# Optimization experiments

Hardware: AMD Instinct MI355X
Metric: run time of the kernel (lower is better)

## Reference

```python
import jax, jax.numpy as jnp
import numpy as np

IN_FEATURES = 3
HIDDEN = 32
NUM_LAYERS = 3
BATCH = 16384
NQ = 128


def setup_inputs() -> dict:
    key = jax.random.key(0)
    ks = jax.random.split(key, 12)
    x = jax.random.normal(ks[0], (BATCH, NQ, IN_FEATURES), dtype=jnp.float32)
    # adjacency with self-loops, row-normalised so each row sums to 1
    a = jax.random.uniform(ks[1], (NQ, NQ), dtype=jnp.float32)
    a = a + jnp.eye(NQ, dtype=jnp.float32)
    adj = a / jnp.sum(a, axis=1, keepdims=True)
    s_lift = 1.0 / np.sqrt(IN_FEATURES)
    s_hid = 1.0 / np.sqrt(HIDDEN)
    W_lift = jax.random.uniform(ks[2], (IN_FEATURES, HIDDEN), jnp.float32, -s_lift, s_lift)
    b_lift = jax.random.uniform(ks[3], (HIDDEN,), jnp.float32, -s_lift, s_lift)
    # stacked per-layer MLP params: [num_layers, ...]
    W1 = jax.random.uniform(ks[4], (NUM_LAYERS, HIDDEN, HIDDEN), jnp.float32, -s_hid, s_hid)
    b1 = jax.random.uniform(ks[5], (NUM_LAYERS, HIDDEN), jnp.float32, -s_hid, s_hid)
    W2 = jax.random.uniform(ks[6], (NUM_LAYERS, HIDDEN, HIDDEN), jnp.float32, -s_hid, s_hid)
    b2 = jax.random.uniform(ks[7], (NUM_LAYERS, HIDDEN), jnp.float32, -s_hid, s_hid)
    W_ro = jax.random.uniform(ks[8], (HIDDEN, 1), jnp.float32, -s_hid, s_hid)
    b_ro = jax.random.uniform(ks[9], (1,), jnp.float32, -s_hid, s_hid)
    return {"x": x, "adj": adj, "W_lift": W_lift, "b_lift": b_lift,
            "W1": W1, "b1": b1, "W2": W2, "b2": b2,
            "W_ro": W_ro, "b_ro": b_ro}


def reference(x, adj, W_lift, b_lift, W1, b1, W2, b2, W_ro, b_ro):
    # lift: [B, N, in] -> [B, N, H]
    h = x @ W_lift + b_lift
    for l in range(W1.shape[0]):  # small fixed layer count
        # local MLP: Linear -> ReLU -> (Dropout: identity at eval) -> Linear
        local = jnp.maximum(h @ W1[l] + b1[l], 0.0) @ W2[l] + b2[l]
        # dense adjacency aggregation: [N,N] x [B,N,H] -> [B,N,H]
        h = jnp.einsum('ij,bjk->bik', adj, local)
    graph_repr = jnp.mean(h, axis=1)  # [B, H]
    return graph_repr @ W_ro + b_ro   # [B, 1]
```

## Files before the change

### kernel.cpp

```cpp
#include <hip/hip_runtime.h>


typedef _Float16 f16;
typedef __attribute__((ext_vector_type(8))) _Float16 half8;
typedef __attribute__((ext_vector_type(4))) _Float16 half4;
typedef __attribute__((ext_vector_type(2))) __fp16 fp16x2;
typedef __attribute__((ext_vector_type(4))) float f32x4;

namespace {
constexpr int N = 128, H = 32;
constexpr int WS_ADJB = 0;
constexpr int WS_W0B  = 32768;
constexpr int WS_MB   = 33792;
constexpr int WS_BIAS = 37888;
constexpr int WS_V    = 38400;
constexpr int WS_U    = 38912;
constexpr int WS_C    = 39040;
}

static __device__ __forceinline__ half4 pk4(float a, float b, float c, float d) {
  union { half4 v; fp16x2 h[2]; } u;
  u.h[0] = __builtin_amdgcn_cvt_pkrtz(a, b);
  u.h[1] = __builtin_amdgcn_cvt_pkrtz(c, d);
  return u.v;
}
static __device__ __forceinline__ half4 relupk(f32x4 c) {
  const half4 z = {};
  return __builtin_elementwise_max(pk4(c[0], c[1], c[2], c[3]), z);
}
static __device__ __forceinline__ half4 pkc(f32x4 c) {
  return pk4(c[0], c[1], c[2], c[3]);
}
static __device__ __forceinline__ half8 cat(half4 lo, half4 hi) {
  return __builtin_shufflevector(lo, hi, 0, 1, 2, 3, 4, 5, 6, 7);
}

#define MF(A, B, C)   __builtin_amdgcn_mfma_f32_16x16x16f16((A), (B), (C), 0, 0, 0)
#define MF32(A, B, C) __builtin_amdgcn_mfma_f32_16x16x32_f16((A), (B), (C), 0, 0, 0)

__global__ void prep(const float* __restrict__ adj,
                     const float* __restrict__ W_lift,
                     const float* __restrict__ b_lift,
                     const float* __restrict__ W1,
                     const float* __restrict__ b1,
                     const float* __restrict__ W2,
                     const float* __restrict__ b2,
                     const float* __restrict__ W_ro,
                     const float* __restrict__ b_ro,
                     char* __restrict__ ws) {
  const int tid = threadIdx.x;
  f16* adjb  = (f16*)(ws + WS_ADJB);
  f16* w0b   = (f16*)(ws + WS_W0B);
  f16* mb    = (f16*)(ws + WS_MB);
  float* bia = (float*)(ws + WS_BIAS);
  float* v   = (float*)(ws + WS_V);
  float* u   = (float*)(ws + WS_U);
  float* cp  = (float*)(ws + WS_C);

  if (blockIdx.x != 0) {
    const int e = (blockIdx.x - 1) * 256 + tid;
    const int gi = e >> 8, c = (e >> 6) & 3, lane = e & 63;
    const int lr = lane & 15, q = lane >> 4;
    const float* src = adj + (gi * 16 + lr) * N + c * 32;
    f16* dst = adjb + e * 8;
#pragma unroll
    for (int j = 0; j < 8; ++j) {
      const int col = (j < 4) ? (4 * q + j) : (12 + 4 * q + j);
      dst[j] = (f16)src[col];
    }
    return;
  }

  __shared__ float tmp[3][H][H];
  __shared__ float vpart[2][N];
  {
    const int c = tid & 127, h = tid >> 7;
    float s = 0.f;
    for (int i = h * 64; i < h * 64 + 64; ++i) s += adj[i * N + c];
    vpart[h][c] = s;
  }
  for (int idx = tid; idx < 3 * H * H; idx += 256) {
    const int l = idx >> 10, rem = idx & 1023;
    const int k = rem >> 5, fo = rem & 31;
    float val = 0.f;
    if (l == 0) {
      if (k < 3) for (int c = 0; c < H; ++c) val += W_lift[k * H + c] * W1[c * H + fo];
    } else {
      const float* w2l = W2 + (l - 1) * H * H;
      const float* w1n = W1 + l * H * H;
      for (int c = 0; c < H; ++c) val += w2l[k * H + c] * w1n[c * H + fo];
    }
    tmp[l][k][fo] = val;
  }
  if (tid < H) {
    float s0 = b1[tid], s1 = b1[H + tid], s2 = b1[2 * H + tid];
    for (int c = 0; c < H; ++c) {
      s0 += b_lift[c] * W1[c * H + tid];
      s1 += b2[c] * W1[H * H + c * H + tid];
      s2 += b2[H + c] * W1[2 * H * H + c * H + tid];
    }
    bia[tid] = s0; bia[H + tid] = s1; bia[2 * H + tid] = s2;
    float su = 0.f;
    for (int c = 0; c < H; ++c) su += W2[2 * H * H + tid * H + c] * W_ro[c];
    u[tid] = su;
  }
  __syncthreads();
  if (tid < N) v[tid] = (vpart[0][tid] + vpart[1][tid]) * (1.0f / N);
  for (int e = tid; e < 512; e += 256) {
    const int t = e >> 8, lane = (e >> 2) & 63, j = e & 3;
    const int lr = lane & 15, q = lane >> 4;
    w0b[e] = (f16)tmp[0][q * 4 + j][t * 16 + lr];
  }
  for (int e = tid; e < 2048; e += 256) {
    const int l = e >> 10, rem = e & 1023;
    const int t = rem >> 9, lane = (rem >> 3) & 63, j = rem & 7;
    const int lr = lane & 15, q = lane >> 4;
    const int k = (j < 4) ? (4 * q + j) : (12 + 4 * q + j);
    mb[e] = (f16)tmp[1 + l][k][t * 16 + lr];
  }
  __syncthreads();
  if (tid < 64) {
    float s = (vpart[0][tid] + vpart[1][tid] + vpart[0][64 + tid] + vpart[1][64 + tid])
              * (1.0f / N);
#pragma unroll
    for (int off = 32; off > 0; off >>= 1) s += __shfl_down(s, off, 64);
    if (tid == 0) {
      float c2r = 0.f;
      for (int k = 0; k < H; ++k) c2r += b2[2 * H + k] * W_ro[k];
      cp[0] = c2r * s + b_ro[0];
    }
  }
}

__global__ __launch_bounds__(256, 2)
void gnn_mfma(const float* __restrict__ x,
              const char* __restrict__ ws,
              float* __restrict__ out) {
  const f16* adjb  = (const f16*)(ws + WS_ADJB);
  const f16* w0b   = (const f16*)(ws + WS_W0B);
  const f16* mb    = (const f16*)(ws + WS_MB);
  const float* bia = (const float*)(ws + WS_BIAS);
  const float* v   = (const float*)(ws + WS_V);
  const float* u   = (const float*)(ws + WS_U);
  const float* cp  = (const float*)(ws + WS_C);

  const int tid  = threadIdx.x;
  const int wave = tid >> 6;
  const int lane = tid & 63;
  const int lrow = lane & 15;
  const int quad = lane >> 4;
  const int b0   = blockIdx.x * 8 + wave * 2;
  const int b1   = b0 + 1;

  const f32x4 zero = {0.f, 0.f, 0.f, 0.f};

  half8 caA0, caA1, caA2, caA3, cbA0, cbA1, cbA2, cbA3;
  half8 caB0, caB1, caB2, caB3, cbB0, cbB1, cbB2, cbB3;
  half8 pfA0, pfA1, pfA2, pfA3, pfA4, pfA5, pfA6, pfA7;
  half8 pfB0, pfB1, pfB2, pfB3, pfB4, pfB5, pfB6, pfB7;

  {
    const half4 w0 = *(const half4*)(w0b + (0 * 64 + lane) * 4);
    const half4 w1 = *(const half4*)(w0b + (1 * 64 + lane) * 4);
    const float bb0 = bia[lrow], bb1 = bia[16 + lrow];
    const f32x4 bi0 = {bb0, bb0, bb0, bb0};
    const f32x4 bi1 = {bb1, bb1, bb1, bb1};
#define L0PAIR(g, CAA, CBA, CAB, CBB)                                        \
    {                                                                        \
      half4 xA0 = {}, xA1 = {}, xB0 = {}, xB1 = {};                          \
      if (quad == 0) {                                                       \
        const float* ra0 = x + ((size_t)b0 * N + (g) * 16 + lrow) * 3;       \
        const float* ra1 = x + ((size_t)b0 * N + ((g) + 1) * 16 + lrow) * 3; \
        const float* rb0 = x + ((size_t)b1 * N + (g) * 16 + lrow) * 3;       \
        const float* rb1 = x + ((size_t)b1 * N + ((g) + 1) * 16 + lrow) * 3; \
        xA0 = pk4(ra0[0], ra0[1], ra0[2], 0.f);                              \
        xA1 = pk4(ra1[0], ra1[1], ra1[2], 0.f);                              \
        xB0 = pk4(rb0[0], rb0[1], rb0[2], 0.f);                              \
        xB1 = pk4(rb1[0], rb1[1], rb1[2], 0.f);                              \
      }                                                                      \
      CAA = cat(relupk(MF(xA0, w0, bi0)), relupk(MF(xA1, w0, bi0)));         \
      CBA = cat(relupk(MF(xA0, w1, bi1)), relupk(MF(xA1, w1, bi1)));         \
      CAB = cat(relupk(MF(xB0, w0, bi0)), relupk(MF(xB1, w0, bi0)));         \
      CBB = cat(relupk(MF(xB0, w1, bi1)), relupk(MF(xB1, w1, bi1)));         \
    }
    L0PAIR(0, caA0, cbA0, caB0, cbB0) L0PAIR(2, caA1, cbA1, caB1, cbB1)
    L0PAIR(4, caA2, cbA2, caB2, cbB2) L0PAIR(6, caA3, cbA3, caB3, cbB3)
#undef L0PAIR
  }

#define GSTEP(gi, PFA, PFB)                                                  \
  {                                                                          \
    f32x4 aA0 = zero, aA1 = zero, aB0 = zero, aB1 = zero;                    \
    const f16* ab = adjb + ((gi) * 256 + lane) * 8;                          \
    half8 bt;                                                                \
    __builtin_amdgcn_s_setprio(1);                                           \
    bt = *(const half8*)(ab + 0 * 512);                                      \
    aA0 = MF32(caA0, bt, aA0); aA1 = MF32(cbA0, bt, aA1);                    \
    aB0 = MF32(caB0, bt, aB0); aB1 = MF32(cbB0, bt, aB1);                    \
    bt = *(const half8*)(ab + 1 * 512);                                      \
    aA0 = MF32(caA1, bt, aA0); aA1 = MF32(cbA1, bt, aA1);                    \
    aB0 = MF32(caB1, bt, aB0); aB1 = MF32(cbB1, bt, aB1);                    \
    bt = *(const half8*)(ab + 2 * 512);                                      \
    aA0 = MF32(caA2, bt, aA0); aA1 = MF32(cbA2, bt, aA1);                    \
    aB0 = MF32(caB2, bt, aB0); aB1 = MF32(cbB2, bt, aB1);                    \
    bt = *(const half8*)(ab + 3 * 512);                                      \
    aA0 = MF32(caA3, bt, aA0); aA1 = MF32(cbA3, bt, aA1);                    \
    aB0 = MF32(caB3, bt, aB0); aB1 = MF32(cbB3, bt, aB1);                    \
    __builtin_amdgcn_s_setprio(0);                                           \
    PFA = cat(pkc(aA0), pkc(aA1));                                           \
    PFB = cat(pkc(aB0), pkc(aB1));                                           \
  }
#define GALL()                                                               \
  GSTEP(0, pfA0, pfB0) GSTEP(1, pfA1, pfB1)                                  \
  __builtin_amdgcn_sched_barrier(0);                                         \
  GSTEP(2, pfA2, pfB2) GSTEP(3, pfA3, pfB3)                                  \
  __builtin_amdgcn_sched_barrier(0);                                         \
  GSTEP(4, pfA4, pfB4) GSTEP(5, pfA5, pfB5)                                  \
  __builtin_amdgcn_sched_barrier(0);                                         \
  GSTEP(6, pfA6, pfB6) GSTEP(7, pfA7, pfB7)

  GALL()

  {
    const f16* mbl = mb + 0 * 1024;
    const half8 m0 = *(const half8*)(mbl + (0 * 64 + lane) * 8);
    const half8 m1 = *(const half8*)(mbl + (1 * 64 + lane) * 8);
    const float bb0 = bia[H + lrow], bb1 = bia[H + 16 + lrow];
    const f32x4 bi0 = {bb0, bb0, bb0, bb0};
    const f32x4 bi1 = {bb1, bb1, bb1, bb1};
#define L1PAIR(PF0, PF1, CA, CB)                                             \
    {                                                                        \
      f32x4 c0a = MF32(PF0, m0, bi0);                                        \
      f32x4 c1a = MF32(PF0, m1, bi1);                                        \
      f32x4 c0b = MF32(PF1, m0, bi0);                                        \
      f32x4 c1b = MF32(PF1, m1, bi1);                                        \
      CA = cat(relupk(c0a), relupk(c0b));                                    \
      CB = cat(relupk(c1a), relupk(c1b));                                    \
    }
    L1PAIR(pfA0, pfA1, caA0, cbA0) L1PAIR(pfB0, pfB1, caB0, cbB0)
    __builtin_amdgcn_sched_barrier(0);
    L1PAIR(pfA2, pfA3, caA1, cbA1) L1PAIR(pfB2, pfB3, caB1, cbB1)
    __builtin_amdgcn_sched_barrier(0);
    L1PAIR(pfA4, pfA5, caA2, cbA2) L1PAIR(pfB4, pfB5, caB2, cbB2)
    __builtin_amdgcn_sched_barrier(0);
    L1PAIR(pfA6, pfA7, caA3, cbA3) L1PAIR(pfB6, pfB7, caB3, cbB3)
#undef L1PAIR
  }

  GALL()
#undef GALL
#undef GSTEP

  {
    const f16* mbl = mb + 1 * 1024;
    const half8 m0 = *(const half8*)(mbl + (0 * 64 + lane) * 8);
    const half8 m1 = *(const half8*)(mbl + (1 * 64 + lane) * 8);
    const float bb0 = bia[2 * H + lrow], bb1 = bia[2 * H + 16 + lrow];
    const f32x4 bi0 = {bb0, bb0, bb0, bb0};
    const f32x4 bi1 = {bb1, bb1, bb1, bb1};
    const float u0 = u[lrow], u1 = u[16 + lrow];
    float pA = 0.f, pB = 0.f;
#define L2G(g, PF, ACC)                                                      \
    {                                                                        \
      f32x4 c0 = MF32(PF, m0, bi0);                                          \
      f32x4 c1 = MF32(PF, m1, bi1);                                          \
      const float4 vv = *(const float4*)(v + (g) * 16 + quad * 4);           \
      ACC += (fmaxf(c0[0], 0.f) * vv.x + fmaxf(c0[1], 0.f) * vv.y +          \
              fmaxf(c0[2], 0.f) * vv.z + fmaxf(c0[3], 0.f) * vv.w) * u0 +    \
             (fmaxf(c1[0], 0.f) * vv.x + fmaxf(c1[1], 0.f) * vv.y +          \
              fmaxf(c1[2], 0.f) * vv.z + fmaxf(c1[3], 0.f) * vv.w) * u1;     \
    }
    L2G(0, pfA0, pA) L2G(0, pfB0, pB) L2G(1, pfA1, pA) L2G(1, pfB1, pB)
    L2G(2, pfA2, pA) L2G(2, pfB2, pB) L2G(3, pfA3, pA) L2G(3, pfB3, pB)
    L2G(4, pfA4, pA) L2G(4, pfB4, pB) L2G(5, pfA5, pA) L2G(5, pfB5, pB)
    L2G(6, pfA6, pA) L2G(6, pfB6, pB) L2G(7, pfA7, pA) L2G(7, pfB7, pB)
#undef L2G
#pragma unroll
    for (int off = 32; off > 0; off >>= 1) {
      pA += __shfl_down(pA, off, 64);
      pB += __shfl_down(pB, off, 64);
    }
    if (lane == 0) {
      out[b0] = pA + cp[0];
      out[b1] = pB + cp[0];
    }
  }
}

extern "C" void kernel_launch(void* const* d_in, const int* in_sizes, int n_in,
                              void* d_out, int out_size, void* d_ws, size_t ws_size,
                              hipStream_t stream) {
  const float* x      = (const float*)d_in[0];
  const float* adj    = (const float*)d_in[1];
  const float* W_lift = (const float*)d_in[2];
  const float* b_lift = (const float*)d_in[3];
  const float* W1     = (const float*)d_in[4];
  const float* b1     = (const float*)d_in[5];
  const float* W2     = (const float*)d_in[6];
  const float* b2     = (const float*)d_in[7];
  const float* W_ro   = (const float*)d_in[8];
  const float* b_ro   = (const float*)d_in[9];
  char* ws = (char*)d_ws;
  float* o = (float*)d_out;

  const int B = in_sizes[0] / (N * 3);
  hipLaunchKernelGGL(prep, dim3(9), dim3(256), 0, stream,
                     adj, W_lift, b_lift, W1, b1, W2, b2, W_ro, b_ro, ws);
  hipLaunchKernelGGL(gnn_mfma, dim3(B / 8), dim3(256), 0, stream,
                     x, (const char*)ws, o);
}
```

Baseline: 138.0 us.

## Double-buffer adjacency tile loads ahead of MFMA groups in aggregation steps

```diff
diff --git a/kernel.cpp b/kernel.cpp
--- a/kernel.cpp
+++ b/kernel.cpp
@@ -37,6 +37,7 @@
 
 #define MF(A, B, C)   __builtin_amdgcn_mfma_f32_16x16x16f16((A), (B), (C), 0, 0, 0)
 #define MF32(A, B, C) __builtin_amdgcn_mfma_f32_16x16x32_f16((A), (B), (C), 0, 0, 0)
+#define SB() __builtin_amdgcn_sched_barrier(0)
 
 __global__ void prep(const float* __restrict__ adj,
                      const float* __restrict__ W_lift,
@@ -158,6 +159,40 @@
   half8 caB0, caB1, caB2, caB3, cbB0, cbB1, cbB2, cbB3;
   half8 pfA0, pfA1, pfA2, pfA3, pfA4, pfA5, pfA6, pfA7;
   half8 pfB0, pfB1, pfB2, pfB3, pfB4, pfB5, pfB6, pfB7;
+  half8 bp0, bp1, bp2, bp3, bq0, bq1, bq2, bq3;
+  half8 mw0, mw1;
+
+#define GLOAD(gi, B0, B1, B2, B3)                                            \
+  {                                                                          \
+    const f16* ab = adjb + ((gi) * 256 + lane) * 8;                          \
+    B0 = *(const half8*)(ab + 0 * 512);                                      \
+    B1 = *(const half8*)(ab + 1 * 512);                                      \
+    B2 = *(const half8*)(ab + 2 * 512);                                      \
+    B3 = *(const half8*)(ab + 3 * 512);                                      \
+  }
+#define GMFMA(B0, B1, B2, B3, PFA, PFB)                                      \
+  {                                                                          \
+    f32x4 aA0 = zero, aA1 = zero, aB0 = zero, aB1 = zero;                    \
+    __builtin_amdgcn_s_setprio(1);                                           \
+    aA0 = MF32(caA0, B0, aA0); aA1 = MF32(cbA0, B0, aA1);                    \
+    aB0 = MF32(caB0, B0, aB0); aB1 = MF32(cbB0, B0, aB1);                    \
+    aA0 = MF32(caA1, B1, aA0); aA1 = MF32(cbA1, B1, aA1);                    \
+    aB0 = MF32(caB1, B1, aB0); aB1 = MF32(cbB1, B1, aB1);                    \
+    aA0 = MF32(caA2, B2, aA0); aA1 = MF32(cbA2, B2, aA1);                    \
+    aB0 = MF32(caB2, B2, aB0); aB1 = MF32(cbB2, B2, aB1);                    \
+    aA0 = MF32(caA3, B3, aA0); aA1 = MF32(cbA3, B3, aA1);                    \
+    aB0 = MF32(caB3, B3, aB0); aB1 = MF32(cbB3, B3, aB1);                    \
+    __builtin_amdgcn_s_setprio(0);                                           \
+    PFA = cat(pkc(aA0), pkc(aA1));                                           \
+    PFB = cat(pkc(aB0), pkc(aB1));                                           \
+  }
+
+  const float cpv = cp[0];
+  const float u0 = u[lrow], u1 = u[16 + lrow];
+  const float bL1a = bia[H + lrow], bL1b = bia[H + 16 + lrow];
+  const float bL2a = bia[2 * H + lrow], bL2b = bia[2 * H + 16 + lrow];
+  GLOAD(0, bp0, bp1, bp2, bp3)
+  GLOAD(1, bq0, bq1, bq2, bq3)
 
   {
     const half4 w0 = *(const half4*)(w0b + (0 * 64 + lane) * 4);
@@ -188,82 +223,63 @@
 #undef L0PAIR
   }
 
-#define GSTEP(gi, PFA, PFB)                                                  \
-  {                                                                          \
-    f32x4 aA0 = zero, aA1 = zero, aB0 = zero, aB1 = zero;                    \
-    const f16* ab = adjb + ((gi) * 256 + lane) * 8;                          \
-    half8 bt;                                                                \
-    __builtin_amdgcn_s_setprio(1);                                           \
-    bt = *(const half8*)(ab + 0 * 512);                                      \
-    aA0 = MF32(caA0, bt, aA0); aA1 = MF32(cbA0, bt, aA1);                    \
-    aB0 = MF32(caB0, bt, aB0); aB1 = MF32(cbB0, bt, aB1);                    \
-    bt = *(const half8*)(ab + 1 * 512);                                      \
-    aA0 = MF32(caA1, bt, aA0); aA1 = MF32(cbA1, bt, aA1);                    \
-    aB0 = MF32(caB1, bt, aB0); aB1 = MF32(cbB1, bt, aB1);                    \
-    bt = *(const half8*)(ab + 2 * 512);                                      \
-    aA0 = MF32(caA2, bt, aA0); aA1 = MF32(cbA2, bt, aA1);                    \
-    aB0 = MF32(caB2, bt, aB0); aB1 = MF32(cbB2, bt, aB1);                    \
-    bt = *(const half8*)(ab + 3 * 512);                                      \
-    aA0 = MF32(caA3, bt, aA0); aA1 = MF32(cbA3, bt, aA1);                    \
-    aB0 = MF32(caB3, bt, aB0); aB1 = MF32(cbB3, bt, aB1);                    \
-    __builtin_amdgcn_s_setprio(0);                                           \
-    PFA = cat(pkc(aA0), pkc(aA1));                                           \
-    PFB = cat(pkc(aB0), pkc(aB1));                                           \
-  }
-#define GALL()                                                               \
-  GSTEP(0, pfA0, pfB0) GSTEP(1, pfA1, pfB1)                                  \
-  __builtin_amdgcn_sched_barrier(0);                                         \
-  GSTEP(2, pfA2, pfB2) GSTEP(3, pfA3, pfB3)                                  \
-  __builtin_amdgcn_sched_barrier(0);                                         \
-  GSTEP(4, pfA4, pfB4) GSTEP(5, pfA5, pfB5)                                  \
-  __builtin_amdgcn_sched_barrier(0);                                         \
-  GSTEP(6, pfA6, pfB6) GSTEP(7, pfA7, pfB7)
-
-  GALL()
-
-  {
-    const f16* mbl = mb + 0 * 1024;
-    const half8 m0 = *(const half8*)(mbl + (0 * 64 + lane) * 8);
-    const half8 m1 = *(const half8*)(mbl + (1 * 64 + lane) * 8);
-    const float bb0 = bia[H + lrow], bb1 = bia[H + 16 + lrow];
-    const f32x4 bi0 = {bb0, bb0, bb0, bb0};
-    const f32x4 bi1 = {bb1, bb1, bb1, bb1};
+  GMFMA(bp0, bp1, bp2, bp3, pfA0, pfB0) GLOAD(2, bp0, bp1, bp2, bp3) SB();
+  GMFMA(bq0, bq1, bq2, bq3, pfA1, pfB1) GLOAD(3, bq0, bq1, bq2, bq3) SB();
+  GMFMA(bp0, bp1, bp2, bp3, pfA2, pfB2) GLOAD(4, bp0, bp1, bp2, bp3) SB();
+  GMFMA(bq0, bq1, bq2, bq3, pfA3, pfB3) GLOAD(5, bq0, bq1, bq2, bq3) SB();
+  GMFMA(bp0, bp1, bp2, bp3, pfA4, pfB4) GLOAD(6, bp0, bp1, bp2, bp3) SB();
+  GMFMA(bq0, bq1, bq2, bq3, pfA5, pfB5) GLOAD(7, bq0, bq1, bq2, bq3) SB();
+  GMFMA(bp0, bp1, bp2, bp3, pfA6, pfB6)
+  {
+    mw0 = *(const half8*)(mb + (0 * 64 + lane) * 8);
+    mw1 = *(const half8*)(mb + (1 * 64 + lane) * 8);
+  } SB();
+  GMFMA(bq0, bq1, bq2, bq3, pfA7, pfB7)
+  GLOAD(0, bp0, bp1, bp2, bp3) GLOAD(1, bq0, bq1, bq2, bq3) SB();
+
+  {
+    const f32x4 bi0 = {bL1a, bL1a, bL1a, bL1a};
+    const f32x4 bi1 = {bL1b, bL1b, bL1b, bL1b};
 #define L1PAIR(PF0, PF1, CA, CB)                                             \
     {                                                                        \
-      f32x4 c0a = MF32(PF0, m0, bi0);                                        \
-      f32x4 c1a = MF32(PF0, m1, bi1);                                        \
-      f32x4 c0b = MF32(PF1, m0, bi0);                                        \
-      f32x4 c1b = MF32(PF1, m1, bi1);                                        \
+      f32x4 c0a = MF32(PF0, mw0, bi0);                                       \
+      f32x4 c1a = MF32(PF0, mw1, bi1);                                       \
+      f32x4 c0b = MF32(PF1, mw0, bi0);                                       \
+      f32x4 c1b = MF32(PF1, mw1, bi1);                                       \
       CA = cat(relupk(c0a), relupk(c0b));                                    \
       CB = cat(relupk(c1a), relupk(c1b));                                    \
     }
-    L1PAIR(pfA0, pfA1, caA0, cbA0) L1PAIR(pfB0, pfB1, caB0, cbB0)
-    __builtin_amdgcn_sched_barrier(0);
-    L1PAIR(pfA2, pfA3, caA1, cbA1) L1PAIR(pfB2, pfB3, caB1, cbB1)
-    __builtin_amdgcn_sched_barrier(0);
-    L1PAIR(pfA4, pfA5, caA2, cbA2) L1PAIR(pfB4, pfB5, caB2, cbB2)
-    __builtin_amdgcn_sched_barrier(0);
-    L1PAIR(pfA6, pfA7, caA3, cbA3) L1PAIR(pfB6, pfB7, caB3, cbB3)
+    L1PAIR(pfA0, pfA1, caA0, cbA0) L1PAIR(pfB0, pfB1, caB0, cbB0) SB();
+    L1PAIR(pfA2, pfA3, caA1, cbA1) L1PAIR(pfB2, pfB3, caB1, cbB1) SB();
+    L1PAIR(pfA4, pfA5, caA2, cbA2) L1PAIR(pfB4, pfB5, caB2, cbB2) SB();
+    L1PAIR(pfA6, pfA7, caA3, cbA3) L1PAIR(pfB6, pfB7, caB3, cbB3) SB();
 #undef L1PAIR
   }
 
-  GALL()
-#undef GALL
-#undef GSTEP
-
-  {
-    const f16* mbl = mb + 1 * 1024;
-    const half8 m0 = *(const half8*)(mbl + (0 * 64 + lane) * 8);
-    const half8 m1 = *(const half8*)(mbl + (1 * 64 + lane) * 8);
-    const float bb0 = bia[2 * H + lrow], bb1 = bia[2 * H + 16 + lrow];
-    const f32x4 bi0 = {bb0, bb0, bb0, bb0};
-    const f32x4 bi1 = {bb1, bb1, bb1, bb1};
-    const float u0 = u[lrow], u1 = u[16 + lrow];
+  GMFMA(bp0, bp1, bp2, bp3, pfA0, pfB0) GLOAD(2, bp0, bp1, bp2, bp3) SB();
+  GMFMA(bq0, bq1, bq2, bq3, pfA1, pfB1) GLOAD(3, bq0, bq1, bq2, bq3) SB();
+  GMFMA(bp0, bp1, bp2, bp3, pfA2, pfB2) GLOAD(4, bp0, bp1, bp2, bp3) SB();
+  GMFMA(bq0, bq1, bq2, bq3, pfA3, pfB3) GLOAD(5, bq0, bq1, bq2, bq3) SB();
+  GMFMA(bp0, bp1, bp2, bp3, pfA4, pfB4) GLOAD(6, bp0, bp1, bp2, bp3) SB();
+  GMFMA(bq0, bq1, bq2, bq3, pfA5, pfB5) GLOAD(7, bq0, bq1, bq2, bq3) SB();
+  GMFMA(bp0, bp1, bp2, bp3, pfA6, pfB6)
+  {
+    mw0 = *(const half8*)(mb + 1024 + (0 * 64 + lane) * 8);
+    mw1 = *(const half8*)(mb + 1024 + (1 * 64 + lane) * 8);
+  } SB();
+  GMFMA(bq0, bq1, bq2, bq3, pfA7, pfB7) SB();
+
+#undef GMFMA
+#undef GLOAD
+
+  {
+    const f32x4 bi0 = {bL2a, bL2a, bL2a, bL2a};
+    const f32x4 bi1 = {bL2b, bL2b, bL2b, bL2b};
     float pA = 0.f, pB = 0.f;
 #define L2G(g, PF, ACC)                                                      \
     {                                                                        \
-      f32x4 c0 = MF32(PF, m0, bi0);                                          \
-      f32x4 c1 = MF32(PF, m1, bi1);                                          \
+      f32x4 c0 = MF32(PF, mw0, bi0);                                         \
+      f32x4 c1 = MF32(PF, mw1, bi1);                                         \
       const float4 vv = *(const float4*)(v + (g) * 16 + quad * 4);           \
       ACC += (fmaxf(c0[0], 0.f) * vv.x + fmaxf(c0[1], 0.f) * vv.y +          \
               fmaxf(c0[2], 0.f) * vv.z + fmaxf(c0[3], 0.f) * vv.w) * u0 +    \
@@ -281,8 +297,8 @@
       pB += __shfl_down(pB, off, 64);
     }
     if (lane == 0) {
-      out[b0] = pA + cp[0];
-      out[b1] = pB + cp[0];
+      out[b0] = pA + cpv;
+      out[b1] = pB + cpv;
     }
   }
 }
```

New measurement: 129.7 us. -6.0%, faster.
